# Kernel optimization log

Hardware: AMD Instinct MI355X
Metric: run time of the kernel (lower is better)

Reference implementation:

```python
import jax, jax.numpy as jnp
import numpy as np

B, NF, G, F, D = 8192, 128, 16, 8, 512


def setup_inputs() -> dict:
    key = jax.random.key(0)
    k1, k2, k3, k4 = jax.random.split(key, 4)
    x = jax.random.normal(k1, (B, NF), dtype=jnp.float32)
    # per-group Linear weights: torch Linear(F, D) weight is [D, F]; store as [G, F, D]
    # init scale ~ 1/sqrt(fan_in) like torch default
    W = jax.random.normal(k2, (G, F, D), dtype=jnp.float32) / np.sqrt(F)
    b = jax.random.normal(k3, (G, D), dtype=jnp.float32) / np.sqrt(F)
    group_idx = jnp.arange(G * F, dtype=jnp.int64).reshape(G, F)  # contiguous groups
    masked_group_idx = jax.random.randint(k4, (B,), 0, G, dtype=jnp.int64)
    return {"x": x, "W": W, "b": b, "group_idx": group_idx,
            "masked_group_idx": masked_group_idx}


def reference(x, W, b, group_idx, masked_group_idx):
    # gather each group's feature columns: [B, G, F]
    xg = x[:, group_idx]
    # batched small GEMMs (block-diagonal gather-GEMM) + bias: [B, G, D]
    out = jnp.einsum('bgf,gfd->bgd', xg, W) + b[None, :, :]
    # zero out the masked group token per batch row
    mask = masked_group_idx[:, None] == jnp.arange(out.shape[1])[None, :]  # [B, G]
    out = jnp.where(mask[:, :, None], jnp.zeros((), out.dtype), out)
    return out
```

## Files before the change

kernel.cpp:

```cpp
#include <hip/hip_runtime.h>
#include <stdint.h>

constexpr int kB  = 8192;
constexpr int kNF = 128;
constexpr int kG  = 16;
constexpr int kF  = 8;
constexpr int kD  = 512;
constexpr int ROWS = 32;
constexpr int BLOCKS = (kB / ROWS) * kG;

__global__ __launch_bounds__(256) void ge_kernel(
    const float* __restrict__ x,
    const float* __restrict__ W,
    const float* __restrict__ bias,
    const int*  __restrict__ mgi_w,
    float* __restrict__ out)
{
    __shared__ float xs[ROWS][kF];
    __shared__ float scale[ROWS];

    const int tid = threadIdx.x;
    const int g   = blockIdx.x & (kG - 1);
    const int b0  = (blockIdx.x >> 4) * ROWS;

    const int lane = tid & 63;
    const int probe = mgi_w[lane];
    const bool lane_ok = (lane & 1) ? (probe == 0)
                                    : (probe >= 0 && probe < kG);
    const unsigned long long bal = __ballot(lane_ok);
    const bool is64 = (bal == ~0ull);

    {
        const int r = tid >> 3;
        const int f = tid & 7;
        xs[r][f] = x[(size_t)(b0 + r) * kNF + g * kF + f];
    }
    if (tid < ROWS) {
        const int b = b0 + tid;
        const int m = mgi_w[is64 ? (2 * b) : b];
        scale[tid] = (m == g) ? 0.0f : 1.0f;
    }

    const int rp   = tid >> 7;
    const int dcol = (tid & 127) << 2;

    float w[kF][4];
    #pragma unroll
    for (int f = 0; f < kF; ++f) {
        *(float4*)&w[f][0] = *(const float4*)(W + ((g * kF + f) * kD + dcol));
    }
    float bz[4];
    *(float4*)&bz[0] = *(const float4*)(bias + (g * kD + dcol));

    __syncthreads();

    float* outp = out + (((size_t)(b0 + rp) * kG + g) * kD + dcol);
    const size_t itstride = (size_t)2 * kG * kD;

    #pragma unroll 4
    for (int it = 0; it < ROWS / 2; ++it) {
        const int r = it * 2 + rp;
        const float s = scale[r];

        float a0 = bz[0], a1 = bz[1], a2 = bz[2], a3 = bz[3];
        #pragma unroll
        for (int f = 0; f < kF; ++f) {
            const float xv = xs[r][f];
            a0 = fmaf(xv, w[f][0], a0);
            a1 = fmaf(xv, w[f][1], a1);
            a2 = fmaf(xv, w[f][2], a2);
            a3 = fmaf(xv, w[f][3], a3);
        }

        float4 o;
        o.x = a0 * s; o.y = a1 * s; o.z = a2 * s; o.w = a3 * s;
        *(float4*)(outp + it * itstride) = o;
    }
}

extern "C" void kernel_launch(void* const* d_in, const int* in_sizes, int n_in,
                              void* d_out, int out_size, void* d_ws, size_t ws_size,
                              hipStream_t stream) {
    const float* x    = (const float*)d_in[0];
    const float* W    = (const float*)d_in[1];
    const float* b    = (const float*)d_in[2];
    const int*   mgi  = (const int*)d_in[4];
    float*       out  = (float*)d_out;

    ge_kernel<<<dim3(BLOCKS), dim3(256), 0, stream>>>(x, W, b, mgi, out);
}
```

Measured before the change: 311.4 us.

## Process all groups per block with double-buffered weight loads

Each block now handles 16 batch rows across all 16 groups instead of 32 rows for one group. The whole x row tile is loaded once with float4 copies, and mask indices are kept in registers. Weights for the next group are prefetched into a second register set while the current group is computed, overlapping W loads with FMAs and stores. The costs are higher register pressure from the two weight buffers, and 8x fewer blocks, each doing more serial work.

```diff
diff --git a/kernel.cpp b/kernel.cpp
--- a/kernel.cpp
+++ b/kernel.cpp
@@ -6,8 +6,48 @@
 constexpr int kG  = 16;
 constexpr int kF  = 8;
 constexpr int kD  = 512;
-constexpr int ROWS = 32;
-constexpr int BLOCKS = (kB / ROWS) * kG;
+constexpr int R   = 16;
+constexpr int BLOCKS = kB / R;
+
+#define GE_LOADW(WREG, BREG, GG)                                              \
+    {                                                                         \
+        _Pragma("unroll")                                                     \
+        for (int f = 0; f < kF; ++f)                                          \
+            *(float4*)WREG[f] =                                               \
+                *(const float4*)(Wd + (size_t)((GG) * kF + f) * kD);          \
+        *(float4*)BREG = *(const float4*)(bd + (size_t)(GG) * kD);            \
+    }
+
+#define GE_COMPUTE(WREG, BREG, GG)                                            \
+    {                                                                         \
+        _Pragma("unroll")                                                     \
+        for (int it = 0; it < R / 2; ++it) {                                  \
+            const int r = 2 * it + rp;                                        \
+            const float4 xv0 = *(const float4*)&xs[r][(GG) * kF];             \
+            const float4 xv1 = *(const float4*)&xs[r][(GG) * kF + 4];         \
+            const float s = (mgr[it] == (GG)) ? 0.0f : 1.0f;                  \
+            float a0 = BREG[0], a1 = BREG[1], a2 = BREG[2], a3 = BREG[3];     \
+            a0 = fmaf(xv0.x, WREG[0][0], a0); a1 = fmaf(xv0.x, WREG[0][1], a1);\
+            a2 = fmaf(xv0.x, WREG[0][2], a2); a3 = fmaf(xv0.x, WREG[0][3], a3);\
+            a0 = fmaf(xv0.y, WREG[1][0], a0); a1 = fmaf(xv0.y, WREG[1][1], a1);\
+            a2 = fmaf(xv0.y, WREG[1][2], a2); a3 = fmaf(xv0.y, WREG[1][3], a3);\
+            a0 = fmaf(xv0.z, WREG[2][0], a0); a1 = fmaf(xv0.z, WREG[2][1], a1);\
+            a2 = fmaf(xv0.z, WREG[2][2], a2); a3 = fmaf(xv0.z, WREG[2][3], a3);\
+            a0 = fmaf(xv0.w, WREG[3][0], a0); a1 = fmaf(xv0.w, WREG[3][1], a1);\
+            a2 = fmaf(xv0.w, WREG[3][2], a2); a3 = fmaf(xv0.w, WREG[3][3], a3);\
+            a0 = fmaf(xv1.x, WREG[4][0], a0); a1 = fmaf(xv1.x, WREG[4][1], a1);\
+            a2 = fmaf(xv1.x, WREG[4][2], a2); a3 = fmaf(xv1.x, WREG[4][3], a3);\
+            a0 = fmaf(xv1.y, WREG[5][0], a0); a1 = fmaf(xv1.y, WREG[5][1], a1);\
+            a2 = fmaf(xv1.y, WREG[5][2], a2); a3 = fmaf(xv1.y, WREG[5][3], a3);\
+            a0 = fmaf(xv1.z, WREG[6][0], a0); a1 = fmaf(xv1.z, WREG[6][1], a1);\
+            a2 = fmaf(xv1.z, WREG[6][2], a2); a3 = fmaf(xv1.z, WREG[6][3], a3);\
+            a0 = fmaf(xv1.w, WREG[7][0], a0); a1 = fmaf(xv1.w, WREG[7][1], a1);\
+            a2 = fmaf(xv1.w, WREG[7][2], a2); a3 = fmaf(xv1.w, WREG[7][3], a3);\
+            float4 o;                                                         \
+            o.x = a0 * s; o.y = a1 * s; o.z = a2 * s; o.w = a3 * s;           \
+            *(float4*)(outp + ((size_t)(2 * it) * kG + (GG)) * kD) = o;       \
+        }                                                                     \
+    }
 
 __global__ __launch_bounds__(256) void ge_kernel(
     const float* __restrict__ x,
@@ -16,65 +56,53 @@
     const int*  __restrict__ mgi_w,
     float* __restrict__ out)
 {
-    __shared__ float xs[ROWS][kF];
-    __shared__ float scale[ROWS];
+    __shared__ __align__(16) float xs[R][kNF];
+    __shared__ int mg[R];
 
     const int tid = threadIdx.x;
-    const int g   = blockIdx.x & (kG - 1);
-    const int b0  = (blockIdx.x >> 4) * ROWS;
+    const int b0  = blockIdx.x * R;
 
     const int lane = tid & 63;
     const int probe = mgi_w[lane];
     const bool lane_ok = (lane & 1) ? (probe == 0)
                                     : (probe >= 0 && probe < kG);
-    const unsigned long long bal = __ballot(lane_ok);
-    const bool is64 = (bal == ~0ull);
+    const bool is64 = (__ballot(lane_ok) == ~0ull);
 
     {
-        const int r = tid >> 3;
-        const int f = tid & 7;
-        xs[r][f] = x[(size_t)(b0 + r) * kNF + g * kF + f];
+        const float4* xsrc = (const float4*)(x + (size_t)b0 * kNF);
+        float4* xdst = (float4*)&xs[0][0];
+        xdst[tid]       = xsrc[tid];
+        xdst[tid + 256] = xsrc[tid + 256];
     }
-    if (tid < ROWS) {
-        const int b = b0 + tid;
-        const int m = mgi_w[is64 ? (2 * b) : b];
-        scale[tid] = (m == g) ? 0.0f : 1.0f;
-    }
+    if (tid < R) mg[tid] = mgi_w[is64 ? 2 * (b0 + tid) : (b0 + tid)];
 
     const int rp   = tid >> 7;
     const int dcol = (tid & 127) << 2;
 
-    float w[kF][4];
-    #pragma unroll
-    for (int f = 0; f < kF; ++f) {
-        *(float4*)&w[f][0] = *(const float4*)(W + ((g * kF + f) * kD + dcol));
-    }
-    float bz[4];
-    *(float4*)&bz[0] = *(const float4*)(bias + (g * kD + dcol));
+    const float* Wd = W + dcol;
+    const float* bd = bias + dcol;
+
+    float wA[kF][4], wB[kF][4];
+    float bA[4], bB[4];
+
+    GE_LOADW(wA, bA, 0)
 
     __syncthreads();
 
-    float* outp = out + (((size_t)(b0 + rp) * kG + g) * kD + dcol);
-    const size_t itstride = (size_t)2 * kG * kD;
+    int mgr[R / 2];
+    #pragma unroll
+    for (int it = 0; it < R / 2; ++it) mgr[it] = mg[2 * it + rp];
 
-    #pragma unroll 4
-    for (int it = 0; it < ROWS / 2; ++it) {
-        const int r = it * 2 + rp;
-        const float s = scale[r];
+    float* outp = out + ((size_t)(b0 + rp) * kG) * kD + dcol;
 
-        float a0 = bz[0], a1 = bz[1], a2 = bz[2], a3 = bz[3];
-        #pragma unroll
-        for (int f = 0; f < kF; ++f) {
-            const float xv = xs[r][f];
-            a0 = fmaf(xv, w[f][0], a0);
-            a1 = fmaf(xv, w[f][1], a1);
-            a2 = fmaf(xv, w[f][2], a2);
-            a3 = fmaf(xv, w[f][3], a3);
+    #pragma unroll 1
+    for (int g = 0; g < kG; g += 2) {
+        GE_LOADW(wB, bB, g + 1)
+        GE_COMPUTE(wA, bA, g)
+        if (g + 2 < kG) {
+            GE_LOADW(wA, bA, g + 2)
         }
-
-        float4 o;
-        o.x = a0 * s; o.y = a1 * s; o.z = a2 * s; o.w = a3 * s;
-        *(float4*)(outp + it * itstride) = o;
+        GE_COMPUTE(wB, bB, g + 1)
     }
 }
 
```

Result: faster. 270.0 us (-13.3%).

## Process all groups per block with per-thread column weights in registers

Applied to the files above, without the earlier changes.

Restructures the grid so each block handles 32 batch rows across all 16 groups, loading the full x rows into shared memory once and holding each thread's column of all group weights and biases in registers. Outputs become scalar coalesced stores per group, and masking uses a select on the stored group index. This removes redundant per-group block setup and weight reloads. The cost is far fewer blocks (256), high register pressure, and narrower stores, which may reduce memory-level parallelism.

```diff
diff --git a/kernel.cpp b/kernel.cpp
--- a/kernel.cpp
+++ b/kernel.cpp
@@ -6,75 +6,72 @@
 constexpr int kG  = 16;
 constexpr int kF  = 8;
 constexpr int kD  = 512;
-constexpr int ROWS = 32;
-constexpr int BLOCKS = (kB / ROWS) * kG;
+constexpr int R   = 32;
+constexpr int THREADS = 512;
+constexpr int BLOCKS  = kB / R;
 
-__global__ __launch_bounds__(256) void ge_kernel(
+__global__ __launch_bounds__(512) void ge_kernel(
     const float* __restrict__ x,
     const float* __restrict__ W,
     const float* __restrict__ bias,
     const int*  __restrict__ mgi_w,
     float* __restrict__ out)
 {
-    __shared__ float xs[ROWS][kF];
-    __shared__ float scale[ROWS];
+    __shared__ __align__(16) float xs[R][kNF];
+    __shared__ int mg[R];
 
     const int tid = threadIdx.x;
-    const int g   = blockIdx.x & (kG - 1);
-    const int b0  = (blockIdx.x >> 4) * ROWS;
+    const int b0  = blockIdx.x * R;
 
     const int lane = tid & 63;
     const int probe = mgi_w[lane];
     const bool lane_ok = (lane & 1) ? (probe == 0)
                                     : (probe >= 0 && probe < kG);
-    const unsigned long long bal = __ballot(lane_ok);
-    const bool is64 = (bal == ~0ull);
+    const bool is64 = (__ballot(lane_ok) == ~0ull);
 
     {
-        const int r = tid >> 3;
-        const int f = tid & 7;
-        xs[r][f] = x[(size_t)(b0 + r) * kNF + g * kF + f];
+        const float4* xsrc = (const float4*)(x + (size_t)b0 * kNF);
+        float4* xdst = (float4*)&xs[0][0];
+        xdst[tid]       = xsrc[tid];
+        xdst[tid + 512] = xsrc[tid + 512];
     }
-    if (tid < ROWS) {
-        const int b = b0 + tid;
-        const int m = mgi_w[is64 ? (2 * b) : b];
-        scale[tid] = (m == g) ? 0.0f : 1.0f;
-    }
+    if (tid < R) mg[tid] = mgi_w[is64 ? 2 * (b0 + tid) : (b0 + tid)];
 
-    const int rp   = tid >> 7;
-    const int dcol = (tid & 127) << 2;
+    float w[kG][kF];
+    #pragma unroll
+    for (int g = 0; g < kG; ++g)
+        #pragma unroll
+        for (int f = 0; f < kF; ++f)
+            w[g][f] = W[(size_t)(g * kF + f) * kD + tid];
 
-    float w[kF][4];
+    float bz[kG];
     #pragma unroll
-    for (int f = 0; f < kF; ++f) {
-        *(float4*)&w[f][0] = *(const float4*)(W + ((g * kF + f) * kD + dcol));
-    }
-    float bz[4];
-    *(float4*)&bz[0] = *(const float4*)(bias + (g * kD + dcol));
+    for (int g = 0; g < kG; ++g)
+        bz[g] = bias[(size_t)g * kD + tid];
 
     __syncthreads();
 
-    float* outp = out + (((size_t)(b0 + rp) * kG + g) * kD + dcol);
-    const size_t itstride = (size_t)2 * kG * kD;
+    float* outp = out + (size_t)b0 * (kG * kD) + tid;
 
-    #pragma unroll 4
-    for (int it = 0; it < ROWS / 2; ++it) {
-        const int r = it * 2 + rp;
-        const float s = scale[r];
-
-        float a0 = bz[0], a1 = bz[1], a2 = bz[2], a3 = bz[3];
+    #pragma unroll 1
+    for (int r = 0; r < R; ++r) {
+        const int m = mg[r];
+        float* orow = outp + (size_t)r * (kG * kD);
         #pragma unroll
-        for (int f = 0; f < kF; ++f) {
-            const float xv = xs[r][f];
-            a0 = fmaf(xv, w[f][0], a0);
-            a1 = fmaf(xv, w[f][1], a1);
-            a2 = fmaf(xv, w[f][2], a2);
-            a3 = fmaf(xv, w[f][3], a3);
+        for (int g = 0; g < kG; ++g) {
+            const float4 xv0 = *(const float4*)&xs[r][g * kF];
+            const float4 xv1 = *(const float4*)&xs[r][g * kF + 4];
+            float a = bz[g];
+            a = fmaf(xv0.x, w[g][0], a);
+            a = fmaf(xv0.y, w[g][1], a);
+            a = fmaf(xv0.z, w[g][2], a);
+            a = fmaf(xv0.w, w[g][3], a);
+            a = fmaf(xv1.x, w[g][4], a);
+            a = fmaf(xv1.y, w[g][5], a);
+            a = fmaf(xv1.z, w[g][6], a);
+            a = fmaf(xv1.w, w[g][7], a);
+            orow[g * kD] = (m == g) ? 0.0f : a;
         }
-
-        float4 o;
-        o.x = a0 * s; o.y = a1 * s; o.z = a2 * s; o.w = a3 * s;
-        *(float4*)(outp + it * itstride) = o;
     }
 }
 
@@ -87,5 +84,5 @@
     const int*   mgi  = (const int*)d_in[4];
     float*       out  = (float*)d_out;
 
-    ge_kernel<<<dim3(BLOCKS), dim3(256), 0, stream>>>(x, W, b, mgi, out);
+    ge_kernel<<<dim3(BLOCKS), dim3(THREADS), 0, stream>>>(x, W, b, mgi, out);
 }
```

Result: slower. 449.5 us (+44.3%).
